# Performance work log

Hardware: AMD Instinct MI355X
Metric: run time of the kernel (lower is better)

Reference implementation:

```python
import jax, jax.numpy as jnp
import numpy as np

HIDDEN = 4096
W = 16          # wave_units
LN_EPS = 1e-5   # torch LayerNorm default


def _layernorm(x, gamma, beta):
    mu = jnp.mean(x, axis=-1, keepdims=True)
    var = jnp.mean(jnp.square(x - mu), axis=-1, keepdims=True)
    return (x - mu) * jax.lax.rsqrt(var + LN_EPS) * gamma + beta


def setup_inputs() -> dict:
    key = jax.random.key(0)
    ks = jax.random.split(key, 12)
    B, S, H = 4, 4096, HIDDEN
    hidden_states = jax.random.normal(ks[0], (B, S, H), dtype=jnp.float32)
    frequencies = jax.random.uniform(ks[1], (W,), dtype=jnp.float32) * 2.0
    phases = jax.random.uniform(ks[2], (W,), dtype=jnp.float32) * (2 * np.pi)
    coupling_raw = jax.random.normal(ks[3], (W, W), dtype=jnp.float32) * 0.1
    mask = jax.random.uniform(ks[4], (W, W)) < 0.75  # coupling_density
    coupling = coupling_raw * mask.astype(jnp.float32)
    damping = jnp.ones((W,), dtype=jnp.float32) * 0.1
    # input_proj: Linear(H, 2W) -> LN -> SiLU -> Linear(2W, W)
    w1 = jax.random.normal(ks[5], (H, 2 * W), dtype=jnp.float32) * 0.02
    b1 = jnp.zeros((2 * W,), dtype=jnp.float32)
    g1 = jnp.ones((2 * W,), dtype=jnp.float32)
    beta1 = jnp.zeros((2 * W,), dtype=jnp.float32)
    w2 = jax.random.normal(ks[6], (2 * W, W), dtype=jnp.float32) * 0.02
    b2 = jnp.zeros((W,), dtype=jnp.float32)
    # output_proj: Linear(W, 2W) -> LN -> SiLU -> Linear(2W, H)
    w3 = jax.random.normal(ks[7], (W, 2 * W), dtype=jnp.float32) * 0.02
    b3 = jnp.zeros((2 * W,), dtype=jnp.float32)
    g2 = jnp.ones((2 * W,), dtype=jnp.float32)
    beta2 = jnp.zeros((2 * W,), dtype=jnp.float32)
    w4 = jax.random.normal(ks[8], (2 * W, H), dtype=jnp.float32) * 0.02
    b4 = jnp.zeros((H,), dtype=jnp.float32)
    time_step = jnp.float32(0.0)  # buffer; incremented by 0.1 each call
    return dict(hidden_states=hidden_states, frequencies=frequencies, phases=phases,
                coupling=coupling, damping=damping,
                w1=w1, b1=b1, g1=g1, beta1=beta1, w2=w2, b2=b2,
                w3=w3, b3=b3, g2=g2, beta2=beta2, w4=w4, b4=b4,
                time_step=time_step)


def reference(hidden_states, frequencies, phases, coupling, damping,
              w1, b1, g1, beta1, w2, b2,
              w3, b3, g2, beta2, w4, b4, time_step):
    x = hidden_states.astype(jnp.float32)  # [B,S,H]
    t = time_step + 0.1
    # input_proj: [B,S,H] -> [B,S,W]
    h = jnp.einsum('bsh,hd->bsd', x, w1) + b1
    h = jax.nn.silu(_layernorm(h, g1, beta1))
    wave_input = jnp.einsum('bsd,dw->bsw', h, w2) + b2
    # base waves are identical for every (b, s): compute once on [W]
    base_waves = jnp.sin(2 * np.pi * frequencies * t + phases) * jnp.exp(-damping * t)
    coupled = jnp.tanh(base_waves @ coupling)  # [W]
    modulated = coupled * (1.0 + wave_input)   # [B,S,W]
    mean_waves = jnp.mean(modulated, axis=(0, 1))  # [W]
    # buffers start at zero: resonance = 0.9*0 + 0.1*|mean_waves|
    resonance = 0.1 * jnp.abs(mean_waves)
    resonance_factor = jax.nn.sigmoid(jnp.mean(resonance))
    # output_proj: [B,S,W] -> [B,S,H]
    o = jnp.einsum('bsw,wd->bsd', modulated, w3) + b3
    o = jax.nn.silu(_layernorm(o, g2, beta2))
    wave_output = jnp.einsum('bsd,dh->bsh', o, w4) + b4
    return hidden_states + wave_output * resonance_factor
```

## Files before the change

kernel.cpp:

```cpp
#include <hip/hip_runtime.h>
#include <hip/hip_bf16.h>
#include <math.h>

#define HID 4096
#define R_TOTAL 16384

typedef __attribute__((ext_vector_type(8))) short short8;
typedef __attribute__((ext_vector_type(8))) unsigned short ushort8;
typedef __attribute__((ext_vector_type(4))) float f32x4;

__device__ __forceinline__ ushort bfc(float f) {
  __hip_bfloat16 h = __float2bfloat16(f);
  return *(ushort*)&h;
}

__global__ __launch_bounds__(256) void wn_prep(
    const float* __restrict__ w1, const float* __restrict__ w4,
    ushort* __restrict__ w1T, ushort* __restrict__ w4T,
    const float* __restrict__ freq, const float* __restrict__ phases,
    const float* __restrict__ coupling, const float* __restrict__ damping,
    const float* __restrict__ tstep, float* __restrict__ cpl,
    float* __restrict__ gacc)
{
  __shared__ ushort tile[64*72];
  __shared__ float base[16];
  const int b = blockIdx.x, t = threadIdx.x;
  if (b < 64) {
    #pragma unroll
    for (int i = 0; i < 8; ++i) {
      const int e = t + i*256, kk = e >> 5, c = e & 31;
      tile[c*72 + kk] = bfc(w1[(size_t)(b*64+kk)*32 + c]);
    }
    __syncthreads();
    const int c = t >> 3, j = t & 7;
    ushort8 v;
    #pragma unroll
    for (int q = 0; q < 8; ++q) v[q] = tile[c*72 + j*8 + q];
    *(ushort8*)&w1T[(size_t)c*HID + b*64 + j*8] = v;
  } else if (b < 128) {
    const int b2 = b - 64;
    #pragma unroll
    for (int i = 0; i < 8; ++i) {
      const int e = t + i*256, d = e >> 6, hh = e & 63;
      tile[hh*40 + d] = bfc(w4[(size_t)d*HID + b2*64 + hh]);
    }
    __syncthreads();
    const int hh = t >> 2, j = t & 3;
    ushort8 v;
    #pragma unroll
    for (int q = 0; q < 8; ++q) v[q] = tile[hh*40 + j*8 + q];
    *(ushort8*)&w4T[(size_t)(b2*64+hh)*32 + j*8] = v;
  } else {
    const float tt = tstep[0] + 0.1f;
    if (t < 16) {
      gacc[t] = 0.f;
      base[t] = sinf(6.283185307179586f*freq[t]*tt + phases[t]) * expf(-damping[t]*tt);
    }
    __syncthreads();
    if (t < 16) {
      float s = 0.f;
      #pragma unroll
      for (int i = 0; i < 16; ++i) s += base[i]*coupling[i*16+t];
      cpl[t] = tanhf(s);
    }
  }
}

__global__ __launch_bounds__(256) void wn_phase1(
    const float* __restrict__ x, const ushort* __restrict__ w1T,
    const float* __restrict__ b1, const float* __restrict__ g1,
    const float* __restrict__ beta1, const float* __restrict__ w2,
    const float* __restrict__ b2, const float* __restrict__ w3,
    const float* __restrict__ b3, const float* __restrict__ g2,
    const float* __restrict__ beta2, const float* __restrict__ cpl,
    ushort* __restrict__ o_ws, float* __restrict__ gacc)
{
  __shared__ __align__(16) float lds[6720];
  ushort* xb  = (ushort*)lds;
  float* red  = lds;
  float* yl   = lds + 4096;
  float* w2l  = lds + 5152;
  float* w3l  = lds + 5664;
  float* msum = lds + 6176;
  const int t  = threadIdx.x;
  const int r0 = blockIdx.x * 32;

  if (t < 128) *(float4*)&w2l[t*4] = *(const float4*)&w2[t*4];
  else { const int u2 = t-128; *(float4*)&w3l[u2*4] = *(const float4*)&w3[u2*4]; }

  const int srow = t >> 3, sc = t & 7;
  const int wg0   = ((sc*2) ^ ((srow&7)<<1));
  const int wbase = srow*128 + wg0*8;
  const float* xp = &x[(size_t)(r0+srow)*HID + sc*16];

  const int w    = t >> 6, l = t & 63;
  const int mt   = w & 1, kh = w >> 1;
  const int lrow = l & 15, lkb = l >> 4;
  const int arow = mt*16 + lrow;
  const int rsw  = (arow&7) << 1;
  const int ra_s0 = arow*128 + ((kh*8 +     lkb) ^ rsw)*8;
  const int ra_s1 = arow*128 + ((kh*8 + 4 + lkb) ^ rsw)*8;
  const ushort* bp0 = &w1T[(size_t)lrow*HID + kh*64 + lkb*8];
  const ushort* bp1 = bp0 + 16*HID;

  f32x4 acc0 = {0.f,0.f,0.f,0.f}, acc1 = {0.f,0.f,0.f,0.f};
  float4 rg0, rg1, rg2, rg3;

  rg0 = *(const float4*)&xp[0];
  rg1 = *(const float4*)&xp[4];
  rg2 = *(const float4*)&xp[8];
  rg3 = *(const float4*)&xp[12];
  {
    ushort8 v0, v1;
    v0[0]=bfc(rg0.x); v0[1]=bfc(rg0.y); v0[2]=bfc(rg0.z); v0[3]=bfc(rg0.w);
    v0[4]=bfc(rg1.x); v0[5]=bfc(rg1.y); v0[6]=bfc(rg1.z); v0[7]=bfc(rg1.w);
    v1[0]=bfc(rg2.x); v1[1]=bfc(rg2.y); v1[2]=bfc(rg2.z); v1[3]=bfc(rg2.w);
    v1[4]=bfc(rg3.x); v1[5]=bfc(rg3.y); v1[6]=bfc(rg3.z); v1[7]=bfc(rg3.w);
    *(ushort8*)&xb[wbase]     = v0;
    *(ushort8*)&xb[wbase + 8] = v1;
  }

  for (int it = 0; it < 32; ++it) {
    const int cur = it & 1;
    if (it < 31) {
      const int kc = (it+1)*128;
      rg0 = *(const float4*)&xp[kc];
      rg1 = *(const float4*)&xp[kc + 4];
      rg2 = *(const float4*)&xp[kc + 8];
      rg3 = *(const float4*)&xp[kc + 12];
    }
    __syncthreads();
    {
      const ushort* xc = &xb[cur*4096];
      const int kg = it*128;
      const short8 av0 = *(const short8*)&xc[ra_s0];
      const short8 bv00 = *(const short8*)(bp0 + kg);
      const short8 bv01 = *(const short8*)(bp1 + kg);
      acc0 = __builtin_amdgcn_mfma_f32_16x16x32_bf16(av0, bv00, acc0, 0, 0, 0);
      acc1 = __builtin_amdgcn_mfma_f32_16x16x32_bf16(av0, bv01, acc1, 0, 0, 0);
      const short8 av1 = *(const short8*)&xc[ra_s1];
      const short8 bv10 = *(const short8*)(bp0 + kg + 32);
      const short8 bv11 = *(const short8*)(bp1 + kg + 32);
      acc0 = __builtin_amdgcn_mfma_f32_16x16x32_bf16(av1, bv10, acc0, 0, 0, 0);
      acc1 = __builtin_amdgcn_mfma_f32_16x16x32_bf16(av1, bv11, acc1, 0, 0, 0);
    }
    __syncthreads();
    if (it < 31) {
      ushort* xn = &xb[(cur^1)*4096];
      ushort8 v0, v1;
      v0[0]=bfc(rg0.x); v0[1]=bfc(rg0.y); v0[2]=bfc(rg0.z); v0[3]=bfc(rg0.w);
      v0[4]=bfc(rg1.x); v0[5]=bfc(rg1.y); v0[6]=bfc(rg1.z); v0[7]=bfc(rg1.w);
      v1[0]=bfc(rg2.x); v1[1]=bfc(rg2.y); v1[2]=bfc(rg2.z); v1[3]=bfc(rg2.w);
      v1[4]=bfc(rg3.x); v1[5]=bfc(rg3.y); v1[6]=bfc(rg3.z); v1[7]=bfc(rg3.w);
      *(ushort8*)&xn[wbase]     = v0;
      *(ushort8*)&xn[wbase + 8] = v1;
    }
  }
  __syncthreads();
  #pragma unroll
  for (int j = 0; j < 4; ++j) {
    red[kh*1056 + (mt*16 + lkb*4 + j)*33 + lrow]      = acc0[j];
    red[kh*1056 + (mt*16 + lkb*4 + j)*33 + 16 + lrow] = acc1[j];
  }
  __syncthreads();
  #pragma unroll
  for (int i = 0; i < 4; ++i) {
    const int e = t + i*256, row = e >> 5, col = e & 31;
    yl[row*33+col] = red[row*33+col] + red[1056 + row*33+col];
  }
  __syncthreads();
  if (t < 128) {
    const int row = t >> 2, q = t & 3, d0 = q*8;
    float v[8]; float mu = 0.f;
    #pragma unroll
    for (int dd = 0; dd < 8; ++dd) { v[dd] = yl[row*33 + d0+dd] + b1[d0+dd]; mu += v[dd]; }
    mu += __shfl_xor(mu,1); mu += __shfl_xor(mu,2); mu *= (1.f/32.f);
    float var = 0.f;
    #pragma unroll
    for (int dd = 0; dd < 8; ++dd) { const float c = v[dd]-mu; var += c*c; }
    var += __shfl_xor(var,1); var += __shfl_xor(var,2);
    const float rs = rsqrtf(var*(1.f/32.f) + 1e-5f);
    float wiv[16];
    #pragma unroll
    for (int ww = 0; ww < 16; ++ww) wiv[ww] = 0.f;
    #pragma unroll
    for (int dd = 0; dd < 8; ++dd) {
      const float hn = (v[dd]-mu)*rs*g1[d0+dd] + beta1[d0+dd];
      const float sl = hn / (1.f + __expf(-hn));
      const float* wr = &w2l[(d0+dd)*16];
      #pragma unroll
      for (int ww = 0; ww < 16; ++ww) wiv[ww] = fmaf(sl, wr[ww], wiv[ww]);
    }
    #pragma unroll
    for (int ww = 0; ww < 16; ++ww) {
      wiv[ww] += __shfl_xor(wiv[ww],1);
      wiv[ww] += __shfl_xor(wiv[ww],2);
    }
    float mod[16];
    #pragma unroll
    for (int ww = 0; ww < 16; ++ww) mod[ww] = cpl[ww]*(1.f + wiv[ww] + b2[ww]);
    #pragma unroll
    for (int j = 0; j < 4; ++j) msum[row*17 + q*4+j] = mod[q*4+j];
    float p[8];
    #pragma unroll
    for (int dd = 0; dd < 8; ++dd) p[dd] = b3[d0+dd];
    #pragma unroll
    for (int ww = 0; ww < 16; ++ww) {
      const float m = mod[ww];
      const float* wr = &w3l[ww*32 + d0];
      #pragma unroll
      for (int dd = 0; dd < 8; ++dd) p[dd] = fmaf(m, wr[dd], p[dd]);
    }
    float mu2 = 0.f;
    #pragma unroll
    for (int dd = 0; dd < 8; ++dd) mu2 += p[dd];
    mu2 += __shfl_xor(mu2,1); mu2 += __shfl_xor(mu2,2); mu2 *= (1.f/32.f);
    float var2 = 0.f;
    #pragma unroll
    for (int dd = 0; dd < 8; ++dd) { const float c = p[dd]-mu2; var2 += c*c; }
    var2 += __shfl_xor(var2,1); var2 += __shfl_xor(var2,2);
    const float rs2 = rsqrtf(var2*(1.f/32.f) + 1e-5f);
    ushort8 ov;
    #pragma unroll
    for (int dd = 0; dd < 8; ++dd) {
      const float hn = (p[dd]-mu2)*rs2*g2[d0+dd] + beta2[d0+dd];
      ov[dd] = bfc(hn / (1.f + __expf(-hn)));
    }
    *(ushort8*)&o_ws[(size_t)(r0+row)*32 + d0] = ov;
  }
  __syncthreads();
  if (t < 16) {
    float s = 0.f;
    for (int r = 0; r < 32; ++r) s += msum[r*17 + t];
    atomicAdd(gacc + t, s);
  }
}

__global__ void wn_phase2(const float* __restrict__ gacc, float* __restrict__ cpl)
{
  __shared__ float res[16];
  const int t = threadIdx.x;
  if (t < 16) res[t] = 0.1f * fabsf(gacc[t] * (1.f/(float)R_TOTAL));
  __syncthreads();
  if (t == 0) {
    float s = 0.f;
    #pragma unroll
    for (int ww = 0; ww < 16; ++ww) s += res[ww];
    cpl[16] = 1.f / (1.f + expf(-s*(1.f/16.f)));
  }
}

__global__ __launch_bounds__(256) void wn_phase3(
    const float* __restrict__ x, const ushort* __restrict__ o_bf,
    const ushort* __restrict__ w4T, const float* __restrict__ b4,
    const float* __restrict__ cpl, float* __restrict__ out)
{
  __shared__ __align__(16) float pl[4][2112];
  const int t = threadIdx.x, l = t & 63, w = t >> 6;
  const int bid = blockIdx.x;
  const int strip = bid & 7;
  const int m0 = (255 - (bid >> 3)) * 64 + w*16;
  const float rf = cpl[16];
  const int lm = l & 15, lkb = l >> 4;
  const short8 bv = *(const short8*)&o_bf[(size_t)(m0+lm)*32 + lkb*8];
  float* myl = pl[w];
  const ushort* wp = &w4T[(size_t)(strip*512 + lm)*32 + lkb*8];
  const int erow = l >> 5;
  const int ecol = (l & 31) * 4;

  for (int c = 0; c < 4; ++c) {
    const int h0 = strip*512 + c*128;
    #pragma unroll
    for (int ntl = 0; ntl < 8; ++ntl) {
      const short8 av = *(const short8*)(wp + (size_t)(c*8 + ntl)*16*32);
      f32x4 cc = {0.f,0.f,0.f,0.f};
      cc = __builtin_amdgcn_mfma_f32_16x16x32_bf16(av, bv, cc, 0, 0, 0);
      *(f32x4*)&myl[lm*132 + ntl*16 + lkb*4] = cc;
    }
    #pragma unroll
    for (int p = 0; p < 8; ++p) {
      const int r = erow + p*2;
      const size_t off = (size_t)(m0 + r)*HID + h0 + ecol;
      const float4 xv  = *(const float4*)&x[off];
      const f32x4 cv  = *(const f32x4*)&myl[r*132 + ecol];
      const float4 bq  = *(const float4*)&b4[h0 + ecol];
      f32x4 s;
      s[0] = fmaf(rf, cv[0] + bq.x, xv.x);
      s[1] = fmaf(rf, cv[1] + bq.y, xv.y);
      s[2] = fmaf(rf, cv[2] + bq.z, xv.z);
      s[3] = fmaf(rf, cv[3] + bq.w, xv.w);
      __builtin_nontemporal_store(s, (f32x4*)&out[off]);
    }
  }
}

extern "C" void kernel_launch(void* const* d_in, const int* in_sizes, int n_in,
                              void* d_out, int out_size, void* d_ws, size_t ws_size,
                              hipStream_t stream) {
  const float* x        = (const float*)d_in[0];
  const float* freq     = (const float*)d_in[1];
  const float* phases   = (const float*)d_in[2];
  const float* coupling = (const float*)d_in[3];
  const float* damping  = (const float*)d_in[4];
  const float* w1       = (const float*)d_in[5];
  const float* b1       = (const float*)d_in[6];
  const float* g1       = (const float*)d_in[7];
  const float* beta1    = (const float*)d_in[8];
  const float* w2       = (const float*)d_in[9];
  const float* b2       = (const float*)d_in[10];
  const float* w3       = (const float*)d_in[11];
  const float* b3       = (const float*)d_in[12];
  const float* g2       = (const float*)d_in[13];
  const float* beta2    = (const float*)d_in[14];
  const float* w4       = (const float*)d_in[15];
  const float* b4       = (const float*)d_in[16];
  const float* tstep    = (const float*)d_in[17];
  float* out = (float*)d_out;

  char* wsb = (char*)d_ws;
  ushort* o_bf = (ushort*)wsb;
  ushort* w1T  = (ushort*)(wsb + (1<<20));
  ushort* w4T  = (ushort*)(wsb + (1<<20) + (256<<10));
  float*  gacc = (float*)(wsb + (1<<20) + (512<<10));
  float*  cpl  = gacc + 16;

  hipLaunchKernelGGL(wn_prep, dim3(129), dim3(256), 0, stream,
                     w1, w4, w1T, w4T, freq, phases, coupling, damping, tstep, cpl, gacc);
  hipLaunchKernelGGL(wn_phase1, dim3(512), dim3(256), 0, stream,
                     x, w1T, b1, g1, beta1, w2, b2, w3, b3, g2, beta2, cpl, o_bf, gacc);
  hipLaunchKernelGGL(wn_phase2, dim3(1), dim3(64), 0, stream, gacc, cpl);
  hipLaunchKernelGGL(wn_phase3, dim3(2048), dim3(256), 0, stream,
                     x, o_bf, w4T, b4, cpl, out);
}
```

Measured before the change: 175.3 us.

## Halve phase1 row tile to 16 rows and split K across four waves

Phase1 now processes 16 rows per block instead of 32 and launches 1024 blocks. Each of the four waves handles a quarter of every 128-wide K chunk rather than a mix of M-half and K-half. The cross-wave reduction becomes a 4-way sum, and LDS use drops to about half. The goal is more blocks and more occupancy to hide latency on the memory-bound read of x, at the cost of fewer MFMAs per barrier, reloading w1T twice as often in total, and more atomics.

```diff
diff --git a/kernel.cpp b/kernel.cpp
--- a/kernel.cpp
+++ b/kernel.cpp
@@ -75,49 +75,41 @@
     const float* __restrict__ beta2, const float* __restrict__ cpl,
     ushort* __restrict__ o_ws, float* __restrict__ gacc)
 {
-  __shared__ __align__(16) float lds[6720];
+  __shared__ __align__(16) float lds[3872];
   ushort* xb  = (ushort*)lds;
   float* red  = lds;
-  float* yl   = lds + 4096;
-  float* w2l  = lds + 5152;
-  float* w3l  = lds + 5664;
-  float* msum = lds + 6176;
+  float* yl   = lds + 2048;
+  float* w2l  = lds + 2576;
+  float* w3l  = lds + 3088;
+  float* msum = lds + 3600;
   const int t  = threadIdx.x;
-  const int r0 = blockIdx.x * 32;
+  const int r0 = blockIdx.x * 16;
 
   if (t < 128) *(float4*)&w2l[t*4] = *(const float4*)&w2[t*4];
   else { const int u2 = t-128; *(float4*)&w3l[u2*4] = *(const float4*)&w3[u2*4]; }
 
-  const int srow = t >> 3, sc = t & 7;
-  const int wg0   = ((sc*2) ^ ((srow&7)<<1));
-  const int wbase = srow*128 + wg0*8;
-  const float* xp = &x[(size_t)(r0+srow)*HID + sc*16];
-
-  const int w    = t >> 6, l = t & 63;
-  const int mt   = w & 1, kh = w >> 1;
+  const int srow = t >> 4, su = t & 15;
+  const int pg    = su ^ ((srow & 7) << 1);
+  const int wbase = srow*128 + pg*8;
+  const float* xp = &x[(size_t)(r0+srow)*HID + su*8];
+
+  const int kh = t >> 6, l = t & 63;
   const int lrow = l & 15, lkb = l >> 4;
-  const int arow = mt*16 + lrow;
-  const int rsw  = (arow&7) << 1;
-  const int ra_s0 = arow*128 + ((kh*8 +     lkb) ^ rsw)*8;
-  const int ra_s1 = arow*128 + ((kh*8 + 4 + lkb) ^ rsw)*8;
-  const ushort* bp0 = &w1T[(size_t)lrow*HID + kh*64 + lkb*8];
+  const int g    = kh*4 + lkb;
+  const int ra   = lrow*128 + (g ^ ((lrow & 7) << 1))*8;
+  const ushort* bp0 = &w1T[(size_t)lrow*HID + kh*32 + lkb*8];
   const ushort* bp1 = bp0 + 16*HID;
 
   f32x4 acc0 = {0.f,0.f,0.f,0.f}, acc1 = {0.f,0.f,0.f,0.f};
-  float4 rg0, rg1, rg2, rg3;
+  float4 rg0, rg1;
 
   rg0 = *(const float4*)&xp[0];
   rg1 = *(const float4*)&xp[4];
-  rg2 = *(const float4*)&xp[8];
-  rg3 = *(const float4*)&xp[12];
   {
-    ushort8 v0, v1;
+    ushort8 v0;
     v0[0]=bfc(rg0.x); v0[1]=bfc(rg0.y); v0[2]=bfc(rg0.z); v0[3]=bfc(rg0.w);
     v0[4]=bfc(rg1.x); v0[5]=bfc(rg1.y); v0[6]=bfc(rg1.z); v0[7]=bfc(rg1.w);
-    v1[0]=bfc(rg2.x); v1[1]=bfc(rg2.y); v1[2]=bfc(rg2.z); v1[3]=bfc(rg2.w);
-    v1[4]=bfc(rg3.x); v1[5]=bfc(rg3.y); v1[6]=bfc(rg3.z); v1[7]=bfc(rg3.w);
-    *(ushort8*)&xb[wbase]     = v0;
-    *(ushort8*)&xb[wbase + 8] = v1;
+    *(ushort8*)&xb[wbase] = v0;
   }
 
   for (int it = 0; it < 32; ++it) {
@@ -126,50 +118,49 @@
       const int kc = (it+1)*128;
       rg0 = *(const float4*)&xp[kc];
       rg1 = *(const float4*)&xp[kc + 4];
-      rg2 = *(const float4*)&xp[kc + 8];
-      rg3 = *(const float4*)&xp[kc + 12];
     }
     __syncthreads();
     {
-      const ushort* xc = &xb[cur*4096];
+      const ushort* xc = &xb[cur*2048];
       const int kg = it*128;
-      const short8 av0 = *(const short8*)&xc[ra_s0];
-      const short8 bv00 = *(const short8*)(bp0 + kg);
-      const short8 bv01 = *(const short8*)(bp1 + kg);
-      acc0 = __builtin_amdgcn_mfma_f32_16x16x32_bf16(av0, bv00, acc0, 0, 0, 0);
-      acc1 = __builtin_amdgcn_mfma_f32_16x16x32_bf16(av0, bv01, acc1, 0, 0, 0);
-      const short8 av1 = *(const short8*)&xc[ra_s1];
-      const short8 bv10 = *(const short8*)(bp0 + kg + 32);
-      const short8 bv11 = *(const short8*)(bp1 + kg + 32);
-      acc0 = __builtin_amdgcn_mfma_f32_16x16x32_bf16(av1, bv10, acc0, 0, 0, 0);
-      acc1 = __builtin_amdgcn_mfma_f32_16x16x32_bf16(av1, bv11, acc1, 0, 0, 0);
+      const short8 av  = *(const short8*)&xc[ra];
+      const short8 bv0 = *(const short8*)(bp0 + kg);
+      const short8 bv1 = *(const short8*)(bp1 + kg);
+      acc0 = __builtin_amdgcn_mfma_f32_16x16x32_bf16(av, bv0, acc0, 0, 0, 0);
+      acc1 = __builtin_amdgcn_mfma_f32_16x16x32_bf16(av, bv1, acc1, 0, 0, 0);
     }
     __syncthreads();
     if (it < 31) {
-      ushort* xn = &xb[(cur^1)*4096];
-      ushort8 v0, v1;
+      ushort* xn = &xb[(cur^1)*2048];
+      ushort8 v0;
       v0[0]=bfc(rg0.x); v0[1]=bfc(rg0.y); v0[2]=bfc(rg0.z); v0[3]=bfc(rg0.w);
       v0[4]=bfc(rg1.x); v0[5]=bfc(rg1.y); v0[6]=bfc(rg1.z); v0[7]=bfc(rg1.w);
-      v1[0]=bfc(rg2.x); v1[1]=bfc(rg2.y); v1[2]=bfc(rg2.z); v1[3]=bfc(rg2.w);
-      v1[4]=bfc(rg3.x); v1[5]=bfc(rg3.y); v1[6]=bfc(rg3.z); v1[7]=bfc(rg3.w);
-      *(ushort8*)&xn[wbase]     = v0;
-      *(ushort8*)&xn[wbase + 8] = v1;
-    }
-  }
-  __syncthreads();
-  #pragma unroll
-  for (int j = 0; j < 4; ++j) {
-    red[kh*1056 + (mt*16 + lkb*4 + j)*33 + lrow]      = acc0[j];
-    red[kh*1056 + (mt*16 + lkb*4 + j)*33 + 16 + lrow] = acc1[j];
-  }
-  __syncthreads();
-  #pragma unroll
-  for (int i = 0; i < 4; ++i) {
-    const int e = t + i*256, row = e >> 5, col = e & 31;
-    yl[row*33+col] = red[row*33+col] + red[1056 + row*33+col];
-  }
-  __syncthreads();
-  if (t < 128) {
+      *(ushort8*)&xn[wbase] = v0;
+    }
+  }
+  __syncthreads();
+  {
+    float* rp = &red[kh*512 + l];
+    #pragma unroll
+    for (int j = 0; j < 4; ++j) { rp[j*64] = acc0[j]; rp[(4+j)*64] = acc1[j]; }
+  }
+  __syncthreads();
+  if (t < 64) {
+    const int rr = (t >> 4)*4, cc = t & 15;
+    #pragma unroll
+    for (int j = 0; j < 4; ++j) {
+      float s0 = 0.f, s1 = 0.f;
+      #pragma unroll
+      for (int k = 0; k < 4; ++k) {
+        s0 += red[k*512 + j*64 + t];
+        s1 += red[k*512 + (4+j)*64 + t];
+      }
+      yl[(rr+j)*33 + cc]      = s0;
+      yl[(rr+j)*33 + 16 + cc] = s1;
+    }
+  }
+  __syncthreads();
+  if (t < 64) {
     const int row = t >> 2, q = t & 3, d0 = q*8;
     float v[8]; float mu = 0.f;
     #pragma unroll
@@ -231,7 +222,7 @@
   __syncthreads();
   if (t < 16) {
     float s = 0.f;
-    for (int r = 0; r < 32; ++r) s += msum[r*17 + t];
+    for (int r = 0; r < 16; ++r) s += msum[r*17 + t];
     atomicAdd(gacc + t, s);
   }
 }
@@ -326,7 +317,7 @@
 
   hipLaunchKernelGGL(wn_prep, dim3(129), dim3(256), 0, stream,
                      w1, w4, w1T, w4T, freq, phases, coupling, damping, tstep, cpl, gacc);
-  hipLaunchKernelGGL(wn_phase1, dim3(512), dim3(256), 0, stream,
+  hipLaunchKernelGGL(wn_phase1, dim3(1024), dim3(256), 0, stream,
                      x, w1T, b1, g1, beta1, w2, b2, w3, b3, g2, beta2, cpl, o_bf, gacc);
   hipLaunchKernelGGL(wn_phase2, dim3(1), dim3(64), 0, stream, gacc, cpl);
   hipLaunchKernelGGL(wn_phase3, dim3(2048), dim3(256), 0, stream,
```

Measured after the change: 168.5 us. -3.9%, faster.
